# Performance work log

Measured on AMD Instinct MI355X. Metric: run time of the kernel, lower is better.

The kernel has to match this reference:

```python
import jax, jax.numpy as jnp
import numpy as np

N_NODES = 50000
N_EDGES = 800000
D_IN = 128
D_OUT = 128


def setup_inputs() -> dict:
    key = jax.random.key(0)
    ks = jax.random.split(key, 10)
    x = jax.random.normal(ks[0], (N_NODES, D_IN), dtype=jnp.float32)
    lp_rows = jax.random.randint(ks[1], (N_EDGES,), 0, N_NODES, dtype=jnp.int32)
    lp_cols = jax.random.randint(ks[2], (N_EDGES,), 0, N_NODES, dtype=jnp.int32)
    # low-pass operator: positive normalized-adjacency-like weights
    lp_vals = jax.random.uniform(ks[3], (N_EDGES,), dtype=jnp.float32) / 16.0
    hp_rows = jax.random.randint(ks[4], (N_EDGES,), 0, N_NODES, dtype=jnp.int32)
    hp_cols = jax.random.randint(ks[5], (N_EDGES,), 0, N_NODES, dtype=jnp.int32)
    # high-pass operator: signed (Laplacian-like) weights
    hp_vals = jax.random.normal(ks[6], (N_EDGES,), dtype=jnp.float32) / 16.0
    alpha_w = jax.random.normal(ks[7], (1, D_IN), dtype=jnp.float32) * 0.05
    alpha_b = jnp.zeros((1,), dtype=jnp.float32)
    W = jax.random.normal(ks[8], (D_OUT, D_IN), dtype=jnp.float32) * (1.0 / np.sqrt(D_IN))
    b = jnp.zeros((D_OUT,), dtype=jnp.float32)
    return {"x": x, "lp_rows": lp_rows, "lp_cols": lp_cols, "lp_vals": lp_vals,
            "hp_rows": hp_rows, "hp_cols": hp_cols, "hp_vals": hp_vals,
            "alpha_w": alpha_w, "alpha_b": alpha_b, "W": W, "b": b}


def _spmm(rows, cols, vals, x, n):
    # COO sparse-dense matmul: out[r] += vals[e] * x[cols[e]]
    return jax.ops.segment_sum(vals[:, None] * x[cols], rows, num_segments=n)


def reference(x, lp_rows, lp_cols, lp_vals, hp_rows, hp_cols, hp_vals,
              alpha_w, alpha_b, W, b):
    n = x.shape[0]
    # per-node mixing gate: alpha_i = sigmoid(x_i . theta + b)  -> [N, 1]
    alpha = jax.nn.sigmoid(x @ alpha_w.T + alpha_b)
    z_lp = _spmm(lp_rows, lp_cols, lp_vals, x, n)   # [N, D_IN]
    z_hp = _spmm(hp_rows, hp_cols, hp_vals, x, n)   # [N, D_IN]
    z_mix = alpha * z_lp + (1.0 - alpha) * z_hp
    out = jax.nn.relu(z_mix @ W.T + b)              # use_activation=True
    return out, alpha
```

## Files before the change

kernel.cpp:

```cpp
#include <hip/hip_runtime.h>

#define N_NODES_C 50000
#define N_EDGES_C 800000
#define N_EDGES2_C (2 * N_EDGES_C)
#define D 128
#define NSHARD 8
#define SCAP 16
#define OFCAP 4096

#define GNODES 64
#define LDP 132
#define GGRID ((N_NODES_C + GNODES - 1) / GNODES)
#define FGRID 2048
#define FEPB ((N_EDGES2_C + FGRID - 1) / FGRID)

static __device__ __forceinline__ unsigned short f2bf(float f) {
  unsigned u = __float_as_uint(f);
  u += 0x7fff + ((u >> 16) & 1);
  return (unsigned short)(u >> 16);
}
static __device__ __forceinline__ float bf_lo(unsigned u) {
  return __uint_as_float(u << 16);
}
static __device__ __forceinline__ float bf_hi(unsigned u) {
  return __uint_as_float(u & 0xffff0000u);
}

static __device__ __forceinline__ int xcd_id() {
  int v;
  asm volatile("s_getreg_b32 %0, hwreg(HW_REG_XCC_ID, 0, 4)" : "=s"(v));
  return v & (NSHARD - 1);
}

__global__ __launch_bounds__(256) void alpha_kernel(
    const float* __restrict__ x,
    const float* __restrict__ aw,
    const float* __restrict__ ab,
    float* __restrict__ alpha_out,
    float* __restrict__ alpha_ws,
    int n) {
  int wave = (int)((blockIdx.x * blockDim.x + threadIdx.x) >> 6);
  int lane = threadIdx.x & 63;
  if (wave >= n) return;
  const float* xr = x + (size_t)wave * D;
  float s = xr[lane] * aw[lane] + xr[lane + 64] * aw[lane + 64];
  #pragma unroll
  for (int off = 32; off > 0; off >>= 1)
    s += __shfl_down(s, off);
  if (lane == 0) {
    float a = 1.0f / (1.0f + __expf(-(s + ab[0])));
    alpha_out[wave] = a;
    alpha_ws[wave] = a;
  }
}

__global__ __launch_bounds__(256) void gemm_kernel(
    const float* __restrict__ x,
    const float* __restrict__ W,
    unsigned* __restrict__ y,
    int n) {
  __shared__ float zs[GNODES][LDP];
  __shared__ float wt[64][LDP];

  int t = threadIdx.x;
  int node0 = blockIdx.x * GNODES;
  int tn = t & 15;
  int tjg = t >> 4;
  int jb = tjg * 4;

  #pragma unroll
  for (int it = 0; it < 8; ++it) {
    int f = t + it * 256;
    int r = f >> 5;
    int c4 = f & 31;
    int node = node0 + r;
    float4 v = make_float4(0.f, 0.f, 0.f, 0.f);
    if (node < n) v = ((const float4*)(x + (size_t)node * D))[c4];
    *(float4*)&zs[r][c4 * 4] = v;
  }

  for (int jh = 0; jh < 2; ++jh) {
    if (jh) __syncthreads();
    #pragma unroll
    for (int it = 0; it < 8; ++it) {
      int f = t + it * 256;
      int j = f >> 5;
      int k4 = f & 31;
      *(float4*)&wt[j][k4 * 4] =
          ((const float4*)W)[(size_t)(jh * 64 + j) * 32 + k4];
    }
    __syncthreads();

    float acc[4][4] = {};
    #pragma unroll 2
    for (int k = 0; k < D; k += 4) {
      float4 w0 = *(const float4*)&wt[jb + 0][k];
      float4 w1 = *(const float4*)&wt[jb + 1][k];
      float4 w2 = *(const float4*)&wt[jb + 2][k];
      float4 w3 = *(const float4*)&wt[jb + 3][k];
      float4 z0 = *(const float4*)&zs[tn][k];
      float4 z1 = *(const float4*)&zs[tn + 16][k];
      float4 z2 = *(const float4*)&zs[tn + 32][k];
      float4 z3 = *(const float4*)&zs[tn + 48][k];
      acc[0][0] += z0.x*w0.x + z0.y*w0.y + z0.z*w0.z + z0.w*w0.w;
      acc[0][1] += z0.x*w1.x + z0.y*w1.y + z0.z*w1.z + z0.w*w1.w;
      acc[0][2] += z0.x*w2.x + z0.y*w2.y + z0.z*w2.z + z0.w*w2.w;
      acc[0][3] += z0.x*w3.x + z0.y*w3.y + z0.z*w3.z + z0.w*w3.w;
      acc[1][0] += z1.x*w0.x + z1.y*w0.y + z1.z*w0.z + z1.w*w0.w;
      acc[1][1] += z1.x*w1.x + z1.y*w1.y + z1.z*w1.z + z1.w*w1.w;
      acc[1][2] += z1.x*w2.x + z1.y*w2.y + z1.z*w2.z + z1.w*w2.w;
      acc[1][3] += z1.x*w3.x + z1.y*w3.y + z1.z*w3.z + z1.w*w3.w;
      acc[2][0] += z2.x*w0.x + z2.y*w0.y + z2.z*w0.z + z2.w*w0.w;
      acc[2][1] += z2.x*w1.x + z2.y*w1.y + z2.z*w1.z + z2.w*w1.w;
      acc[2][2] += z2.x*w2.x + z2.y*w2.y + z2.z*w2.z + z2.w*w2.w;
      acc[2][3] += z2.x*w3.x + z2.y*w3.y + z2.z*w3.z + z2.w*w3.w;
      acc[3][0] += z3.x*w0.x + z3.y*w0.y + z3.z*w0.z + z3.w*w0.w;
      acc[3][1] += z3.x*w1.x + z3.y*w1.y + z3.z*w1.z + z3.w*w1.w;
      acc[3][2] += z3.x*w2.x + z3.y*w2.y + z3.z*w2.z + z3.w*w2.w;
      acc[3][3] += z3.x*w3.x + z3.y*w3.y + z3.z*w3.z + z3.w*w3.w;
    }

    #pragma unroll
    for (int ii = 0; ii < 4; ++ii) {
      int node = node0 + ii * 16 + tn;
      if (node < n) {
        uint2 o;
        o.x = (unsigned)f2bf(acc[ii][0]) | ((unsigned)f2bf(acc[ii][1]) << 16);
        o.y = (unsigned)f2bf(acc[ii][2]) | ((unsigned)f2bf(acc[ii][3]) << 16);
        *(uint2*)&y[(size_t)node * 64 + jh * 32 + tjg * 2] = o;
      }
    }
  }
}

__global__ __launch_bounds__(256) void fill_kernel(
    const int* __restrict__ lp_rows, const int* __restrict__ lp_cols,
    const float* __restrict__ lp_vals,
    const int* __restrict__ hp_rows, const int* __restrict__ hp_cols,
    const float* __restrict__ hp_vals,
    const float* __restrict__ alpha,
    int* __restrict__ rcursor,
    unsigned* __restrict__ pairs,
    int* __restrict__ ofcnt,
    uint2* __restrict__ ofl) {
  int xcc = xcd_id();
  int t = threadIdx.x;
  int e0 = blockIdx.x * FEPB;
  int e1 = e0 + FEPB;
  if (e1 > N_EDGES2_C) e1 = N_EDGES2_C;
  for (int e = e0 + t; e < e1; e += 256) {
    int r, c;
    float v;
    if (e < N_EDGES_C) {
      r = lp_rows[e];
      c = lp_cols[e];
      v = lp_vals[e] * alpha[r];
    } else {
      int i = e - N_EDGES_C;
      r = hp_rows[i];
      c = hp_cols[i];
      v = hp_vals[i] * (1.0f - alpha[r]);
    }
    int p = atomicAdd(&rcursor[xcc * N_NODES_C + r], 1);
    if (p < SCAP) {
      unsigned pk = (unsigned)c | ((unsigned)f2bf(v) << 16);
      pairs[((size_t)r << 7) + (xcc << 4) + p] = pk;
    } else {
      int q = atomicAdd(ofcnt, 1);
      if (q < OFCAP)
        ofl[q] = make_uint2(((unsigned)r << 16) | (unsigned)c,
                            (unsigned)__float_as_int(v));
    }
  }
}

__global__ __launch_bounds__(256) void gather_kernel(
    const int* __restrict__ rcursor,
    const unsigned* __restrict__ pairs,
    const unsigned* __restrict__ y,
    const float* __restrict__ bias,
    const int* __restrict__ ofcnt,
    const uint2* __restrict__ ofl,
    float* __restrict__ out) {
  __shared__ float2 part[4][64];
  int t = threadIdx.x;
  int w = t >> 6;
  int lane = t & 63;
  int row = blockIdx.x * 2 + (w >> 1);
  int half = w & 1;

  float aL = 0.f, aH = 0.f;
  if (row < N_NODES_C) {
    const unsigned* rp = pairs + ((size_t)row << 7) + (half << 6);
    unsigned wsrc = rp[lane];

    #pragma unroll
    for (int sc = 0; sc < 4; ++sc) {
      int s = half * 4 + sc;
      int ds = rcursor[(size_t)s * N_NODES_C + row];
      if (ds > SCAP) ds = SCAP;
      int base = sc << 4;
      int p = 0;
      for (; p + 1 < ds; p += 2) {
        unsigned pk0 = (unsigned)__shfl((int)wsrc, base + p);
        unsigned pk1 = (unsigned)__shfl((int)wsrc, base + p + 1);
        unsigned u0 = y[(size_t)(pk0 & 0xffffu) * 64 + lane];
        unsigned u1 = y[(size_t)(pk1 & 0xffffu) * 64 + lane];
        float v0 = bf_hi(pk0);
        float v1 = bf_hi(pk1);
        aL += v0 * bf_lo(u0) + v1 * bf_lo(u1);
        aH += v0 * bf_hi(u0) + v1 * bf_hi(u1);
      }
      if (p < ds) {
        unsigned pk = (unsigned)__shfl((int)wsrc, base + p);
        unsigned u = y[(size_t)(pk & 0xffffu) * 64 + lane];
        aL += bf_hi(pk) * bf_lo(u);
        aH += bf_hi(pk) * bf_hi(u);
      }
    }

    if (half == 0) {
      int nof = *ofcnt;
      if (nof > OFCAP) nof = OFCAP;
      for (int i = 0; i < nof; ++i) {
        uint2 o = ofl[i];
        if ((int)(o.x >> 16) == row) {
          unsigned u = y[(size_t)(o.x & 0xffffu) * 64 + lane];
          float v = __int_as_float((int)o.y);
          aL += v * bf_lo(u);
          aH += v * bf_hi(u);
        }
      }
    }
  }
  part[w][lane] = make_float2(aL, aH);
  __syncthreads();

  if (half == 0 && row < N_NODES_C) {
    float2 a = part[w][lane];
    float2 b = part[w + 1][lane];
    float2 bv = *(const float2*)&bias[lane * 2];
    float2 o;
    o.x = fmaxf(a.x + b.x + bv.x, 0.0f);
    o.y = fmaxf(a.y + b.y + bv.y, 0.0f);
    *(float2*)&out[(size_t)row * D + lane * 2] = o;
  }
}

extern "C" void kernel_launch(void* const* d_in, const int* in_sizes, int n_in,
                              void* d_out, int out_size, void* d_ws, size_t ws_size,
                              hipStream_t stream) {
  const float* x = (const float*)d_in[0];
  const int* lp_rows = (const int*)d_in[1];
  const int* lp_cols = (const int*)d_in[2];
  const float* lp_vals = (const float*)d_in[3];
  const int* hp_rows = (const int*)d_in[4];
  const int* hp_cols = (const int*)d_in[5];
  const float* hp_vals = (const float*)d_in[6];
  const float* alpha_w = (const float*)d_in[7];
  const float* alpha_b = (const float*)d_in[8];
  const float* W = (const float*)d_in[9];
  const float* bias = (const float*)d_in[10];

  float* out = (float*)d_out;
  float* alpha_out = out + (size_t)N_NODES_C * D;

  char* ws = (char*)d_ws;
  unsigned* y = (unsigned*)ws;   ws += (size_t)N_NODES_C * 64 * 4;
  float* alpha_ws = (float*)ws;  ws += 200192;
  int* rcursor = (int*)ws;       ws += (size_t)N_NODES_C * NSHARD * 4;
  int* ofcnt = (int*)ws;         ws += 256;
  uint2* ofl = (uint2*)ws;       ws += (size_t)OFCAP * 8;
  unsigned* pairs = (unsigned*)ws;
  ws += (size_t)N_NODES_C * NSHARD * SCAP * 4;

  hipMemsetAsync(rcursor, 0,
                 (size_t)N_NODES_C * NSHARD * sizeof(int) + 256, stream);

  alpha_kernel<<<(N_NODES_C + 3) / 4, 256, 0, stream>>>(
      x, alpha_w, alpha_b, alpha_out, alpha_ws, N_NODES_C);

  gemm_kernel<<<GGRID, 256, 0, stream>>>(x, W, y, N_NODES_C);

  fill_kernel<<<FGRID, 256, 0, stream>>>(
      lp_rows, lp_cols, lp_vals, hp_rows, hp_cols, hp_vals,
      alpha_ws, rcursor, pairs, ofcnt, ofl);

  gather_kernel<<<(N_NODES_C + 1) / 2, 256, 0, stream>>>(
      rcursor, pairs, (const unsigned*)y, bias, ofcnt, ofl, out);
}
```

Baseline: 314.8 us.

## Fuse GEMM and edge-fill into one interleaved launch, fold cursor zeroing into alpha

Merges the dense x·W^T GEMM and the edge bucketing fill into one kernel. Blocks are interleaved so GEMM tiles and fill chunks run side by side, letting compute-heavy and atomic-heavy work overlap. The hipMemsetAsync of the cursors is moved into the alpha kernel. Edge-index loads now use nontemporal hints. This removes two launches and a memset. The tradeoff is that fill blocks now carry the GEMM's large LDS allocation, which can reduce occupancy.

```diff
diff --git a/kernel.cpp b/kernel.cpp
--- a/kernel.cpp
+++ b/kernel.cpp
@@ -13,6 +13,7 @@
 #define GGRID ((N_NODES_C + GNODES - 1) / GNODES)
 #define FGRID 2048
 #define FEPB ((N_EDGES2_C + FGRID - 1) / FGRID)
+#define TOTG (GGRID + FGRID)
 
 static __device__ __forceinline__ unsigned short f2bf(float f) {
   unsigned u = __float_as_uint(f);
@@ -32,14 +33,18 @@
   return v & (NSHARD - 1);
 }
 
-__global__ __launch_bounds__(256) void alpha_kernel(
+__global__ __launch_bounds__(256) void alpha_zero_kernel(
     const float* __restrict__ x,
     const float* __restrict__ aw,
     const float* __restrict__ ab,
     float* __restrict__ alpha_out,
     float* __restrict__ alpha_ws,
+    int* __restrict__ rcursor,
     int n) {
-  int wave = (int)((blockIdx.x * blockDim.x + threadIdx.x) >> 6);
+  int gtid = blockIdx.x * blockDim.x + threadIdx.x;
+  if (gtid < NSHARD * N_NODES_C + 64) rcursor[gtid] = 0;
+
+  int wave = gtid >> 6;
   int lane = threadIdx.x & 63;
   if (wave >= n) return;
   const float* xr = x + (size_t)wave * D;
@@ -54,86 +59,10 @@
   }
 }
 
-__global__ __launch_bounds__(256) void gemm_kernel(
+__global__ __launch_bounds__(256) void gemm_fill_kernel(
     const float* __restrict__ x,
     const float* __restrict__ W,
     unsigned* __restrict__ y,
-    int n) {
-  __shared__ float zs[GNODES][LDP];
-  __shared__ float wt[64][LDP];
-
-  int t = threadIdx.x;
-  int node0 = blockIdx.x * GNODES;
-  int tn = t & 15;
-  int tjg = t >> 4;
-  int jb = tjg * 4;
-
-  #pragma unroll
-  for (int it = 0; it < 8; ++it) {
-    int f = t + it * 256;
-    int r = f >> 5;
-    int c4 = f & 31;
-    int node = node0 + r;
-    float4 v = make_float4(0.f, 0.f, 0.f, 0.f);
-    if (node < n) v = ((const float4*)(x + (size_t)node * D))[c4];
-    *(float4*)&zs[r][c4 * 4] = v;
-  }
-
-  for (int jh = 0; jh < 2; ++jh) {
-    if (jh) __syncthreads();
-    #pragma unroll
-    for (int it = 0; it < 8; ++it) {
-      int f = t + it * 256;
-      int j = f >> 5;
-      int k4 = f & 31;
-      *(float4*)&wt[j][k4 * 4] =
-          ((const float4*)W)[(size_t)(jh * 64 + j) * 32 + k4];
-    }
-    __syncthreads();
-
-    float acc[4][4] = {};
-    #pragma unroll 2
-    for (int k = 0; k < D; k += 4) {
-      float4 w0 = *(const float4*)&wt[jb + 0][k];
-      float4 w1 = *(const float4*)&wt[jb + 1][k];
-      float4 w2 = *(const float4*)&wt[jb + 2][k];
-      float4 w3 = *(const float4*)&wt[jb + 3][k];
-      float4 z0 = *(const float4*)&zs[tn][k];
-      float4 z1 = *(const float4*)&zs[tn + 16][k];
-      float4 z2 = *(const float4*)&zs[tn + 32][k];
-      float4 z3 = *(const float4*)&zs[tn + 48][k];
-      acc[0][0] += z0.x*w0.x + z0.y*w0.y + z0.z*w0.z + z0.w*w0.w;
-      acc[0][1] += z0.x*w1.x + z0.y*w1.y + z0.z*w1.z + z0.w*w1.w;
-      acc[0][2] += z0.x*w2.x + z0.y*w2.y + z0.z*w2.z + z0.w*w2.w;
-      acc[0][3] += z0.x*w3.x + z0.y*w3.y + z0.z*w3.z + z0.w*w3.w;
-      acc[1][0] += z1.x*w0.x + z1.y*w0.y + z1.z*w0.z + z1.w*w0.w;
-      acc[1][1] += z1.x*w1.x + z1.y*w1.y + z1.z*w1.z + z1.w*w1.w;
-      acc[1][2] += z1.x*w2.x + z1.y*w2.y + z1.z*w2.z + z1.w*w2.w;
-      acc[1][3] += z1.x*w3.x + z1.y*w3.y + z1.z*w3.z + z1.w*w3.w;
-      acc[2][0] += z2.x*w0.x + z2.y*w0.y + z2.z*w0.z + z2.w*w0.w;
-      acc[2][1] += z2.x*w1.x + z2.y*w1.y + z2.z*w1.z + z2.w*w1.w;
-      acc[2][2] += z2.x*w2.x + z2.y*w2.y + z2.z*w2.z + z2.w*w2.w;
-      acc[2][3] += z2.x*w3.x + z2.y*w3.y + z2.z*w3.z + z2.w*w3.w;
-      acc[3][0] += z3.x*w0.x + z3.y*w0.y + z3.z*w0.z + z3.w*w0.w;
-      acc[3][1] += z3.x*w1.x + z3.y*w1.y + z3.z*w1.z + z3.w*w1.w;
-      acc[3][2] += z3.x*w2.x + z3.y*w2.y + z3.z*w2.z + z3.w*w2.w;
-      acc[3][3] += z3.x*w3.x + z3.y*w3.y + z3.z*w3.z + z3.w*w3.w;
-    }
-
-    #pragma unroll
-    for (int ii = 0; ii < 4; ++ii) {
-      int node = node0 + ii * 16 + tn;
-      if (node < n) {
-        uint2 o;
-        o.x = (unsigned)f2bf(acc[ii][0]) | ((unsigned)f2bf(acc[ii][1]) << 16);
-        o.y = (unsigned)f2bf(acc[ii][2]) | ((unsigned)f2bf(acc[ii][3]) << 16);
-        *(uint2*)&y[(size_t)node * 64 + jh * 32 + tjg * 2] = o;
-      }
-    }
-  }
-}
-
-__global__ __launch_bounds__(256) void fill_kernel(
     const int* __restrict__ lp_rows, const int* __restrict__ lp_cols,
     const float* __restrict__ lp_vals,
     const int* __restrict__ hp_rows, const int* __restrict__ hp_cols,
@@ -142,34 +71,114 @@
     int* __restrict__ rcursor,
     unsigned* __restrict__ pairs,
     int* __restrict__ ofcnt,
-    uint2* __restrict__ ofl) {
-  int xcc = xcd_id();
+    uint2* __restrict__ ofl,
+    int n) {
+  __shared__ float zs[GNODES][LDP];
+  __shared__ float wt[64][LDP];
+
   int t = threadIdx.x;
-  int e0 = blockIdx.x * FEPB;
-  int e1 = e0 + FEPB;
-  if (e1 > N_EDGES2_C) e1 = N_EDGES2_C;
-  for (int e = e0 + t; e < e1; e += 256) {
-    int r, c;
-    float v;
-    if (e < N_EDGES_C) {
-      r = lp_rows[e];
-      c = lp_cols[e];
-      v = lp_vals[e] * alpha[r];
-    } else {
-      int i = e - N_EDGES_C;
-      r = hp_rows[i];
-      c = hp_cols[i];
-      v = hp_vals[i] * (1.0f - alpha[r]);
-    }
-    int p = atomicAdd(&rcursor[xcc * N_NODES_C + r], 1);
-    if (p < SCAP) {
-      unsigned pk = (unsigned)c | ((unsigned)f2bf(v) << 16);
-      pairs[((size_t)r << 7) + (xcc << 4) + p] = pk;
-    } else {
-      int q = atomicAdd(ofcnt, 1);
-      if (q < OFCAP)
-        ofl[q] = make_uint2(((unsigned)r << 16) | (unsigned)c,
-                            (unsigned)__float_as_int(v));
+  int bid = blockIdx.x;
+  int g = (bid * GGRID) / TOTG;
+  int gn = ((bid + 1) * GGRID) / TOTG;
+
+  if (gn > g) {
+    int node0 = g * GNODES;
+    int tn = t & 15;
+    int tjg = t >> 4;
+    int jb = tjg * 4;
+
+    #pragma unroll
+    for (int it = 0; it < 8; ++it) {
+      int f = t + it * 256;
+      int r = f >> 5;
+      int c4 = f & 31;
+      int node = node0 + r;
+      float4 v = make_float4(0.f, 0.f, 0.f, 0.f);
+      if (node < n) v = ((const float4*)(x + (size_t)node * D))[c4];
+      *(float4*)&zs[r][c4 * 4] = v;
+    }
+
+    for (int jh = 0; jh < 2; ++jh) {
+      if (jh) __syncthreads();
+      #pragma unroll
+      for (int it = 0; it < 8; ++it) {
+        int f = t + it * 256;
+        int j = f >> 5;
+        int k4 = f & 31;
+        *(float4*)&wt[j][k4 * 4] =
+            ((const float4*)W)[(size_t)(jh * 64 + j) * 32 + k4];
+      }
+      __syncthreads();
+
+      float acc[4][4] = {};
+      #pragma unroll 2
+      for (int k = 0; k < D; k += 4) {
+        float4 w0 = *(const float4*)&wt[jb + 0][k];
+        float4 w1 = *(const float4*)&wt[jb + 1][k];
+        float4 w2 = *(const float4*)&wt[jb + 2][k];
+        float4 w3 = *(const float4*)&wt[jb + 3][k];
+        float4 z0 = *(const float4*)&zs[tn][k];
+        float4 z1 = *(const float4*)&zs[tn + 16][k];
+        float4 z2 = *(const float4*)&zs[tn + 32][k];
+        float4 z3 = *(const float4*)&zs[tn + 48][k];
+        acc[0][0] += z0.x*w0.x + z0.y*w0.y + z0.z*w0.z + z0.w*w0.w;
+        acc[0][1] += z0.x*w1.x + z0.y*w1.y + z0.z*w1.z + z0.w*w1.w;
+        acc[0][2] += z0.x*w2.x + z0.y*w2.y + z0.z*w2.z + z0.w*w2.w;
+        acc[0][3] += z0.x*w3.x + z0.y*w3.y + z0.z*w3.z + z0.w*w3.w;
+        acc[1][0] += z1.x*w0.x + z1.y*w0.y + z1.z*w0.z + z1.w*w0.w;
+        acc[1][1] += z1.x*w1.x + z1.y*w1.y + z1.z*w1.z + z1.w*w1.w;
+        acc[1][2] += z1.x*w2.x + z1.y*w2.y + z1.z*w2.z + z1.w*w2.w;
+        acc[1][3] += z1.x*w3.x + z1.y*w3.y + z1.z*w3.z + z1.w*w3.w;
+        acc[2][0] += z2.x*w0.x + z2.y*w0.y + z2.z*w0.z + z2.w*w0.w;
+        acc[2][1] += z2.x*w1.x + z2.y*w1.y + z2.z*w1.z + z2.w*w1.w;
+        acc[2][2] += z2.x*w2.x + z2.y*w2.y + z2.z*w2.z + z2.w*w2.w;
+        acc[2][3] += z2.x*w3.x + z2.y*w3.y + z2.z*w3.z + z2.w*w3.w;
+        acc[3][0] += z3.x*w0.x + z3.y*w0.y + z3.z*w0.z + z3.w*w0.w;
+        acc[3][1] += z3.x*w1.x + z3.y*w1.y + z3.z*w1.z + z3.w*w1.w;
+        acc[3][2] += z3.x*w2.x + z3.y*w2.y + z3.z*w2.z + z3.w*w2.w;
+        acc[3][3] += z3.x*w3.x + z3.y*w3.y + z3.z*w3.z + z3.w*w3.w;
+      }
+
+      #pragma unroll
+      for (int ii = 0; ii < 4; ++ii) {
+        int node = node0 + ii * 16 + tn;
+        if (node < n) {
+          uint2 o;
+          o.x = (unsigned)f2bf(acc[ii][0]) | ((unsigned)f2bf(acc[ii][1]) << 16);
+          o.y = (unsigned)f2bf(acc[ii][2]) | ((unsigned)f2bf(acc[ii][3]) << 16);
+          *(uint2*)&y[(size_t)node * 64 + jh * 32 + tjg * 2] = o;
+        }
+      }
+    }
+  } else {
+    int fb = bid - g;
+    int xcc = xcd_id();
+    int e0 = fb * FEPB;
+    int e1 = e0 + FEPB;
+    if (e1 > N_EDGES2_C) e1 = N_EDGES2_C;
+    for (int e = e0 + t; e < e1; e += 256) {
+      int r, c;
+      float v;
+      if (e < N_EDGES_C) {
+        r = __builtin_nontemporal_load(lp_rows + e);
+        c = __builtin_nontemporal_load(lp_cols + e);
+        v = __builtin_nontemporal_load(lp_vals + e) * alpha[r];
+      } else {
+        int i = e - N_EDGES_C;
+        r = __builtin_nontemporal_load(hp_rows + i);
+        c = __builtin_nontemporal_load(hp_cols + i);
+        v = __builtin_nontemporal_load(hp_vals + i) * (1.0f - alpha[r]);
+      }
+      int p = atomicAdd(&rcursor[xcc * N_NODES_C + r], 1);
+      if (p < SCAP) {
+        unsigned pk = (unsigned)c | ((unsigned)f2bf(v) << 16);
+        pairs[((size_t)r << 7) + (xcc << 4) + p] = pk;
+      } else {
+        int q = atomicAdd(ofcnt, 1);
+        if (q < OFCAP)
+          ofl[q] = make_uint2(((unsigned)r << 16) | (unsigned)c,
+                              (unsigned)__float_as_int(v));
+      }
     }
   }
 }
@@ -274,17 +283,13 @@
   unsigned* pairs = (unsigned*)ws;
   ws += (size_t)N_NODES_C * NSHARD * SCAP * 4;
 
-  hipMemsetAsync(rcursor, 0,
-                 (size_t)N_NODES_C * NSHARD * sizeof(int) + 256, stream);
-
-  alpha_kernel<<<(N_NODES_C + 3) / 4, 256, 0, stream>>>(
-      x, alpha_w, alpha_b, alpha_out, alpha_ws, N_NODES_C);
-
-  gemm_kernel<<<GGRID, 256, 0, stream>>>(x, W, y, N_NODES_C);
-
-  fill_kernel<<<FGRID, 256, 0, stream>>>(
+  alpha_zero_kernel<<<(N_NODES_C + 3) / 4, 256, 0, stream>>>(
+      x, alpha_w, alpha_b, alpha_out, alpha_ws, rcursor, N_NODES_C);
+
+  gemm_fill_kernel<<<TOTG, 256, 0, stream>>>(
+      x, W, y,
       lp_rows, lp_cols, lp_vals, hp_rows, hp_cols, hp_vals,
-      alpha_ws, rcursor, pairs, ofcnt, ofl);
+      alpha_ws, rcursor, pairs, ofcnt, ofl, N_NODES_C);
 
   gather_kernel<<<(N_NODES_C + 1) / 2, 256, 0, stream>>>(
       rcursor, pairs, (const unsigned*)y, bias, ofcnt, ofl, out);
```

Measured after the change: 296.5 us. -5.8%, faster.
